# Kernel optimization log

Hardware: AMD Instinct MI355X
Metric: run time of the kernel (lower is better)

Reference implementation:

```python
import jax, jax.numpy as jnp
import numpy as np

TEMP = 0.5  # matches init_kwargs temperature


def setup_inputs() -> dict:
    key = jax.random.key(0)
    k1, k2 = jax.random.split(key)
    B, D = 4096, 256
    return {
        "z_i": jax.random.normal(k1, (B, D), dtype=jnp.float32),
        "z_j": jax.random.normal(k2, (B, D), dtype=jnp.float32),
    }


def reference(z_i, z_j):
    B = z_i.shape[0]
    N = 2 * B
    z = jnp.concatenate([z_i, z_j], axis=0)          # [N, D]
    sim = (z @ z.T) / TEMP                            # [N, N]

    # Faithful to source: BOTH positive halves come from diag(sim, +B)
    pos = jnp.concatenate([jnp.diagonal(sim, offset=B)] * 2)  # [N]

    # Arithmetic mask: exclude diagonal and the +/-B off-diagonals (static)
    idx = np.arange(N)
    mask = (idx[:, None] != idx[None, :]) & (np.abs(idx[:, None] - idx[None, :]) != B)
    neg = jnp.where(jnp.asarray(mask), sim, -jnp.inf)          # [N, N]

    # logits = [pos | negatives], label = 0 -> CE_i = lse(logits_i) - pos_i
    logits = jnp.concatenate([pos[:, None], neg], axis=1)      # [N, N+1]
    lse = jax.nn.logsumexp(logits, axis=1)                     # [N]
    loss = jnp.mean(lse - pos) / N                             # CE mean, then /N as in source
    return loss
```

## Files before the change

### kernel.cpp

```cpp
#include <hip/hip_runtime.h>
#include <hip/hip_bf16.h>

#define DD 256
#define NN 8192
#define B_ROWS 4096
#define NRG 32
#define NCJ 64
#define NBLK 1056
#define M_FIX 160.0f
#define SCALE 1.6986436f
#define LN2 0.69314718055994531f

typedef __attribute__((ext_vector_type(8))) short bf16x8;
typedef __attribute__((ext_vector_type(4))) float f32x4;

__device__ __forceinline__ unsigned short f2bf(float f) {
    unsigned int x = __float_as_uint(f);
    x += 0x7fffu + ((x >> 16) & 1u);
    return (unsigned short)(x >> 16);
}
__device__ __forceinline__ float bf2f(unsigned short u) {
    return __uint_as_float((unsigned int)u << 16);
}
__device__ __forceinline__ float exp2_raw(float x) {
    float r; asm("v_exp_f32 %0, %1" : "=v"(r) : "v"(x)); return r;
}
__device__ __forceinline__ void gload16(const unsigned short* g, unsigned short* l) {
    __builtin_amdgcn_global_load_lds(
        (const __attribute__((address_space(1))) void*)g,
        (__attribute__((address_space(3))) void*)l, 16, 0, 0);
}

__global__ void cast_pos_kernel(const float* __restrict__ zi, const float* __restrict__ zj,
                                unsigned short* __restrict__ zb, float* __restrict__ pos) {
    const int w = threadIdx.x >> 6;
    const int l = threadIdx.x & 63;
    const int r = blockIdx.x * 4 + w;
    const float4 a = ((const float4*)(zi + (size_t)r * DD))[l];
    const float4 b = ((const float4*)(zj + (size_t)r * DD))[l];
    float d = a.x * b.x + a.y * b.y + a.z * b.z + a.w * b.w;
    #pragma unroll
    for (int off = 32; off > 0; off >>= 1) d += __shfl_down(d, off, 64);
    if (l == 0) pos[r] = 2.0f * d;
    ushort4 oa, ob;
    oa.x = f2bf(a.x * SCALE); oa.y = f2bf(a.y * SCALE);
    oa.z = f2bf(a.z * SCALE); oa.w = f2bf(a.w * SCALE);
    ob.x = f2bf(b.x * SCALE); ob.y = f2bf(b.y * SCALE);
    ob.z = f2bf(b.z * SCALE); ob.w = f2bf(b.w * SCALE);
    ((ushort4*)(zb + (size_t)r * DD))[l] = oa;
    ((ushort4*)(zb + (size_t)(r + B_ROWS) * DD))[l] = ob;
}

__global__ __launch_bounds__(256, 2) void simlse_kernel(const unsigned short* __restrict__ zb,
                                                        unsigned short* __restrict__ PT) {
    __shared__ unsigned short tile[2][16 * 512];
    const int tid = threadIdx.x;
    const int w  = tid >> 6;
    const int l  = tid & 63;
    const int lg = l >> 4;
    const int lr = l & 15;

    const int wg = ((int)blockIdx.x & 7) * (NBLK / 8) + ((int)blockIdx.x >> 3);
    int b = wg, rg = 0;
    while (b >= NCJ - 2 * rg) { b -= NCJ - 2 * rg; ++rg; }
    const int cj = 2 * rg + b;
    const bool mirror = (cj >= 2 * rg + 2);
    const int rbase = rg * 256 + w * 64;
    const int cbase = cj * 128;
    const int ri_u0 = rg * 16 + w * 4;

    bf16x8 aF[4][8];
    #pragma unroll
    for (int rt = 0; rt < 4; ++rt) {
        const unsigned short* ap = zb + (size_t)(rbase + rt * 16 + lr) * DD + lg * 8;
        #pragma unroll
        for (int ks = 0; ks < 8; ++ks) aF[rt][ks] = *(const bf16x8*)(ap + ks * 32);
    }

    float rs[4][4];
    #pragma unroll
    for (int rt = 0; rt < 4; ++rt)
        #pragma unroll
        for (int j = 0; j < 4; ++j) rs[rt][j] = 0.f;
    float cs[8];
    #pragma unroll
    for (int ct = 0; ct < 8; ++ct) cs[ct] = 0.f;

    #pragma unroll
    for (int jj = 0; jj < 4; ++jj) {
        const int slot = w * 4 + jj, sl = slot >> 3, ks = slot & 7;
        gload16(zb + (size_t)(cbase + sl * 16 + lr) * DD + ks * 32 + lg * 8,
                &tile[0][slot * 512]);
    }
    __syncthreads();

    for (int c = 0; c < 4; ++c) {
        if (c < 3) {
            const int c1 = cbase + (c + 1) * 32;
            #pragma unroll
            for (int jj = 0; jj < 4; ++jj) {
                const int slot = w * 4 + jj, sl = slot >> 3, ks = slot & 7;
                gload16(zb + (size_t)(c1 + sl * 16 + lr) * DD + ks * 32 + lg * 8,
                        &tile[(c + 1) & 1][slot * 512]);
            }
        }
        const unsigned short* buf = tile[c & 1];
        #pragma unroll
        for (int sl = 0; sl < 2; ++sl) {
            const int ct = c * 2 + sl;
            f32x4 acc[4];
            #pragma unroll
            for (int rt = 0; rt < 4; ++rt) acc[rt] = (f32x4){0.f, 0.f, 0.f, 0.f};
            #pragma unroll
            for (int ks = 0; ks < 8; ++ks) {
                bf16x8 bF = *(const bf16x8*)(buf + (sl * 8 + ks) * 512 + l * 8);
                #pragma unroll
                for (int rt = 0; rt < 4; ++rt)
                    acc[rt] = __builtin_amdgcn_mfma_f32_16x16x32_bf16(aF[rt][ks], bF, acc[rt], 0, 0, 0);
            }
            const int ci_u = cj * 8 + ct;
            #pragma unroll
            for (int rt = 0; rt < 4; ++rt) {
                const bool dt = (!mirror) && (ri_u0 + rt == ci_u);
                #pragma unroll
                for (int j = 0; j < 4; ++j) {
                    float e = exp2_raw(acc[rt][j] - M_FIX);
                    if (dt && (lr == lg * 4 + j)) e = 0.f;
                    rs[rt][j] += e;
                    cs[ct] += e;
                }
            }
        }
        __syncthreads();
    }

    #pragma unroll
    for (int rt = 0; rt < 4; ++rt)
        #pragma unroll
        for (int j = 0; j < 4; ++j) {
            float v = rs[rt][j];
            v += __shfl_xor(v, 1, 64);
            v += __shfl_xor(v, 2, 64);
            v += __shfl_xor(v, 4, 64);
            v += __shfl_xor(v, 8, 64);
            rs[rt][j] = v;
        }
    if (lr == 0) {
        #pragma unroll
        for (int rt = 0; rt < 4; ++rt)
            #pragma unroll
            for (int j = 0; j < 4; ++j)
                PT[(size_t)cj * NN + rbase + rt * 16 + lg * 4 + j] = f2bf(rs[rt][j]);
    }

    if (mirror) {
        #pragma unroll
        for (int ct = 0; ct < 8; ++ct) {
            float v = cs[ct];
            v += __shfl_xor(v, 16, 64);
            v += __shfl_xor(v, 32, 64);
            cs[ct] = v;
        }
        float* red = (float*)tile;
        if (lg == 0) {
            #pragma unroll
            for (int ct = 0; ct < 8; ++ct) red[w * 128 + ct * 16 + lr] = cs[ct];
        }
        __syncthreads();
        if (tid < 128) {
            const float v = red[tid] + red[128 + tid] + red[256 + tid] + red[384 + tid];
            PT[(size_t)(2 * rg) * NN + cbase + tid] = f2bf(v);
        }
    }
}

__global__ void rowmerge_kernel(const unsigned short* __restrict__ PT,
                                const float* __restrict__ pos, float* __restrict__ partial) {
    const int r = blockIdx.x * 256 + threadIdx.x;
    const int rg = r >> 8;
    float S = 0.f;
    for (int s = 2 * rg; s < NCJ; ++s) S += bf2f(PT[(size_t)s * NN + r]);
    for (int s = 0; s < 2 * rg; s += 2) S += bf2f(PT[(size_t)s * NN + r]);
    float val = M_FIX * LN2 + logf(S);
    if (r < B_ROWS) val -= 2.0f * pos[r];
    __shared__ float red[256];
    red[threadIdx.x] = val;
    __syncthreads();
    for (int st = 128; st > 0; st >>= 1) {
        if (threadIdx.x < st) red[threadIdx.x] += red[threadIdx.x + st];
        __syncthreads();
    }
    if (threadIdx.x == 0) partial[blockIdx.x] = red[0];
}

__global__ void final_kernel(const float* __restrict__ partial, float* __restrict__ out) {
    float v = (threadIdx.x < 32) ? partial[threadIdx.x] : 0.f;
    #pragma unroll
    for (int off = 32; off > 0; off >>= 1) v += __shfl_down(v, off, 64);
    if (threadIdx.x == 0) out[0] = v / (8192.f * 8192.f);
}

extern "C" void kernel_launch(void* const* d_in, const int* in_sizes, int n_in,
                              void* d_out, int out_size, void* d_ws, size_t ws_size,
                              hipStream_t stream) {
    const float* zi = (const float*)d_in[0];
    const float* zj = (const float*)d_in[1];
    float* out = (float*)d_out;
    char* ws = (char*)d_ws;

    unsigned short* zb = (unsigned short*)ws;
    unsigned short* PT = (unsigned short*)(ws + (size_t)NN * DD * 2);
    float* pos     = (float*)(ws + (size_t)NN * DD * 2 + (size_t)NCJ * NN * 2);
    float* partial = pos + B_ROWS;

    hipLaunchKernelGGL(cast_pos_kernel, dim3(B_ROWS / 4), dim3(256), 0, stream, zi, zj, zb, pos);
    hipLaunchKernelGGL(simlse_kernel,   dim3(NBLK), dim3(256), 0, stream, zb, PT);
    hipLaunchKernelGGL(rowmerge_kernel, dim3(NN / 256), dim3(256), 0, stream, PT, pos, partial);
    hipLaunchKernelGGL(final_kernel,    dim3(1), dim3(64), 0, stream, partial, out);
}
```

Before: 70.90 us.

## Load whole column tile to LDS upfront and widen rowmerge parallelism

The sim/LSE kernel now issues all column-tile global-to-LDS loads at the start, before loading the A fragments, into a single 64KB buffer. This replaces the double-buffered four-chunk loop and its per-chunk barriers with one barrier. The aim is to overlap the B loads with the A-fragment register loads and remove synchronisation. The cost is LDS use growing from 32KB to 64KB per block, which may limit occupancy to two blocks per CU. The rowmerge kernel uses 128-thread blocks, giving 64 blocks, and a fully unrolled, predicated loop over all 64 partial slots. The final reduce now reads all 64 partials.

```diff
diff --git a/kernel.cpp b/kernel.cpp
--- a/kernel.cpp
+++ b/kernel.cpp
@@ -53,7 +53,7 @@
 
 __global__ __launch_bounds__(256, 2) void simlse_kernel(const unsigned short* __restrict__ zb,
                                                         unsigned short* __restrict__ PT) {
-    __shared__ unsigned short tile[2][16 * 512];
+    __shared__ unsigned short tile[64 * 512];
     const int tid = threadIdx.x;
     const int w  = tid >> 6;
     const int l  = tid & 63;
@@ -69,6 +69,13 @@
     const int cbase = cj * 128;
     const int ri_u0 = rg * 16 + w * 4;
 
+    #pragma unroll
+    for (int jj = 0; jj < 16; ++jj) {
+        const int slot = w * 16 + jj, sl = slot >> 3, ks = slot & 7;
+        gload16(zb + (size_t)(cbase + sl * 16 + lr) * DD + ks * 32 + lg * 8,
+                tile + slot * 512);
+    }
+
     bf16x8 aF[4][8];
     #pragma unroll
     for (int rt = 0; rt < 4; ++rt) {
@@ -86,52 +93,33 @@
     #pragma unroll
     for (int ct = 0; ct < 8; ++ct) cs[ct] = 0.f;
 
-    #pragma unroll
-    for (int jj = 0; jj < 4; ++jj) {
-        const int slot = w * 4 + jj, sl = slot >> 3, ks = slot & 7;
-        gload16(zb + (size_t)(cbase + sl * 16 + lr) * DD + ks * 32 + lg * 8,
-                &tile[0][slot * 512]);
-    }
     __syncthreads();
 
-    for (int c = 0; c < 4; ++c) {
-        if (c < 3) {
-            const int c1 = cbase + (c + 1) * 32;
-            #pragma unroll
-            for (int jj = 0; jj < 4; ++jj) {
-                const int slot = w * 4 + jj, sl = slot >> 3, ks = slot & 7;
-                gload16(zb + (size_t)(c1 + sl * 16 + lr) * DD + ks * 32 + lg * 8,
-                        &tile[(c + 1) & 1][slot * 512]);
+    #pragma unroll
+    for (int sl = 0; sl < 8; ++sl) {
+        f32x4 acc[4];
+        #pragma unroll
+        for (int rt = 0; rt < 4; ++rt)
+            acc[rt] = (f32x4){0.f, 0.f, 0.f, 0.f};
+        #pragma unroll
+        for (int ks = 0; ks < 8; ++ks) {
+            bf16x8 bF = *(const bf16x8*)(tile + (sl * 8 + ks) * 512 + l * 8);
+            #pragma unroll
+            for (int rt = 0; rt < 4; ++rt)
+                acc[rt] = __builtin_amdgcn_mfma_f32_16x16x32_bf16(aF[rt][ks], bF, acc[rt], 0, 0, 0);
+        }
+        const int ci_u = cj * 8 + sl;
+        #pragma unroll
+        for (int rt = 0; rt < 4; ++rt) {
+            const bool dt = (!mirror) && (ri_u0 + rt == ci_u);
+            #pragma unroll
+            for (int j = 0; j < 4; ++j) {
+                float e = exp2_raw(acc[rt][j] - M_FIX);
+                if (dt && (lr == lg * 4 + j)) e = 0.f;
+                rs[rt][j] += e;
+                cs[sl] += e;
             }
         }
-        const unsigned short* buf = tile[c & 1];
-        #pragma unroll
-        for (int sl = 0; sl < 2; ++sl) {
-            const int ct = c * 2 + sl;
-            f32x4 acc[4];
-            #pragma unroll
-            for (int rt = 0; rt < 4; ++rt) acc[rt] = (f32x4){0.f, 0.f, 0.f, 0.f};
-            #pragma unroll
-            for (int ks = 0; ks < 8; ++ks) {
-                bf16x8 bF = *(const bf16x8*)(buf + (sl * 8 + ks) * 512 + l * 8);
-                #pragma unroll
-                for (int rt = 0; rt < 4; ++rt)
-                    acc[rt] = __builtin_amdgcn_mfma_f32_16x16x32_bf16(aF[rt][ks], bF, acc[rt], 0, 0, 0);
-            }
-            const int ci_u = cj * 8 + ct;
-            #pragma unroll
-            for (int rt = 0; rt < 4; ++rt) {
-                const bool dt = (!mirror) && (ri_u0 + rt == ci_u);
-                #pragma unroll
-                for (int j = 0; j < 4; ++j) {
-                    float e = exp2_raw(acc[rt][j] - M_FIX);
-                    if (dt && (lr == lg * 4 + j)) e = 0.f;
-                    rs[rt][j] += e;
-                    cs[ct] += e;
-                }
-            }
-        }
-        __syncthreads();
     }
 
     #pragma unroll
@@ -161,6 +149,7 @@
             v += __shfl_xor(v, 32, 64);
             cs[ct] = v;
         }
+        __syncthreads();
         float* red = (float*)tile;
         if (lg == 0) {
             #pragma unroll
@@ -174,19 +163,24 @@
     }
 }
 
-__global__ void rowmerge_kernel(const unsigned short* __restrict__ PT,
-                                const float* __restrict__ pos, float* __restrict__ partial) {
-    const int r = blockIdx.x * 256 + threadIdx.x;
+__global__ __launch_bounds__(128) void rowmerge_kernel(const unsigned short* __restrict__ PT,
+                                                       const float* __restrict__ pos,
+                                                       float* __restrict__ partial) {
+    const int r = blockIdx.x * 128 + threadIdx.x;
     const int rg = r >> 8;
     float S = 0.f;
-    for (int s = 2 * rg; s < NCJ; ++s) S += bf2f(PT[(size_t)s * NN + r]);
-    for (int s = 0; s < 2 * rg; s += 2) S += bf2f(PT[(size_t)s * NN + r]);
+    #pragma unroll
+    for (int s = 0; s < NCJ; ++s) {
+        const float v = bf2f(PT[(size_t)s * NN + r]);
+        const bool valid = (s >= 2 * rg) || ((s & 1) == 0);
+        S += valid ? v : 0.f;
+    }
     float val = M_FIX * LN2 + logf(S);
     if (r < B_ROWS) val -= 2.0f * pos[r];
-    __shared__ float red[256];
+    __shared__ float red[128];
     red[threadIdx.x] = val;
     __syncthreads();
-    for (int st = 128; st > 0; st >>= 1) {
+    for (int st = 64; st > 0; st >>= 1) {
         if (threadIdx.x < st) red[threadIdx.x] += red[threadIdx.x + st];
         __syncthreads();
     }
@@ -194,7 +188,7 @@
 }
 
 __global__ void final_kernel(const float* __restrict__ partial, float* __restrict__ out) {
-    float v = (threadIdx.x < 32) ? partial[threadIdx.x] : 0.f;
+    float v = partial[threadIdx.x];
     #pragma unroll
     for (int off = 32; off > 0; off >>= 1) v += __shfl_down(v, off, 64);
     if (threadIdx.x == 0) out[0] = v / (8192.f * 8192.f);
@@ -215,6 +209,6 @@
 
     hipLaunchKernelGGL(cast_pos_kernel, dim3(B_ROWS / 4), dim3(256), 0, stream, zi, zj, zb, pos);
     hipLaunchKernelGGL(simlse_kernel,   dim3(NBLK), dim3(256), 0, stream, zb, PT);
-    hipLaunchKernelGGL(rowmerge_kernel, dim3(NN / 256), dim3(256), 0, stream, PT, pos, partial);
+    hipLaunchKernelGGL(rowmerge_kernel, dim3(NN / 128), dim3(128), 0, stream, PT, pos, partial);
     hipLaunchKernelGGL(final_kernel,    dim3(1), dim3(64), 0, stream, partial, out);
 }
```

After: 62.55 us. -11.8%, faster.
